# Performance work log

Measured on AMD Instinct MI355X. Metric: run time of the kernel, lower is better.

The kernel has to match this reference:

```python
import jax, jax.numpy as jnp
import numpy as np

B, L, H, NH, HD, M, NL, V, RD, NS = 4, 512, 768, 12, 64, 3072, 6, 32000, 128, 2
EPS = 1e-12
COEF = 1.0 / float(np.sqrt(HD))
NEG_INF = float('-inf')


def _ln(x, scale, bias):
    x = x - jnp.mean(x, axis=-1, keepdims=True)
    x = x * jax.lax.rsqrt(jnp.mean(jnp.square(x), axis=-1, keepdims=True) + EPS)
    return x * scale + bias


def setup_inputs() -> dict:
    key = jax.random.key(0)
    ks = jax.random.split(key, 16)
    def p(k, shape):
        return jax.random.normal(k, shape, jnp.float32) * 0.02
    return dict(
        token_ids=jax.random.randint(ks[0], (B, L), 0, V, jnp.int32),
        segment_ids=jax.random.randint(ks[1], (B, L), 0, NS, jnp.int32),
        input_mask=jnp.ones((B, L), jnp.int32),
        tok_emb=p(ks[2], (V, H)),
        seg_emb=p(ks[3], (NS, H)),
        emb_scale=jnp.ones((H,), jnp.float32),
        emb_bias=jnp.zeros((H,), jnp.float32),
        Wq=p(ks[4], (NL, H, NH, HD)), bq=jnp.zeros((NL, NH, HD), jnp.float32),
        Wk=p(ks[5], (NL, H, NH, HD)), bk=jnp.zeros((NL, NH, HD), jnp.float32),
        Wv=p(ks[6], (NL, H, NH, HD)), bv=jnp.zeros((NL, NH, HD), jnp.float32),
        relpos=p(ks[7], (NL, 2 * RD - 1, H)),
        Wo=p(ks[8], (NL, NH, HD, H)), bo=jnp.zeros((NL, H), jnp.float32),
        ln1_s=jnp.ones((NL, H), jnp.float32), ln1_b=jnp.zeros((NL, H), jnp.float32),
        W1=p(ks[9], (NL, H, M)), b1=jnp.zeros((NL, M), jnp.float32),
        W2=p(ks[10], (NL, M, H)), b2=jnp.zeros((NL, H), jnp.float32),
        ln2_s=jnp.ones((NL, H), jnp.float32), ln2_b=jnp.zeros((NL, H), jnp.float32),
    )


def _encoder(token_ids, segment_ids, input_mask,
             tok_emb, seg_emb, emb_scale, emb_bias,
             Wq, bq, Wk, bk, Wv, bv, relpos, Wo, bo,
             ln1_s, ln1_b, W1, b1, W2, b2, ln2_s, ln2_b):
    # Embedding block: token + segment embeddings, layer norm (dropout = eval/no-op)
    x = tok_emb[token_ids] + seg_emb[segment_ids]            # [B, L, H]
    x = _ln(x, emb_scale, emb_bias)
    mask = jnp.where(input_mask.astype(bool), 0.0, NEG_INF)[:, None, None, :]  # [B,1,1,L]

    for i in range(NL):
        # --- relative-position self-attention ---
        q = jnp.einsum('bqe,ehd->bqhd', x, Wq[i]) + bq[i]
        k = jnp.einsum('bke,ehd->bkhd', x, Wk[i]) + bk[i]
        v = jnp.einsum('bke,ehd->bkhd', x, Wv[i]) + bv[i]
        att = jnp.einsum('bqhd,bkhd->bhqk', q, k) + mask      # [B,NH,L,L]
        # skew trick: embed absolute [L,L] scores into relative [L, 2L-1] layout
        att = jnp.pad(att, [(0, 0), (0, 0), (0, 0), (0, L - 2)], constant_values=NEG_INF)
        att = att.reshape(att.shape[:2] + (L * (2 * L - 2),))
        att = jnp.pad(att, [(0, 0), (0, 0), (L - 1, 1)], constant_values=NEG_INF)
        att = att.reshape(att.shape[:2] + (L, 2 * L - 1))     # [B,NH,L,2L-1]
        # relative-position key/value embeddings, edge-padded to 2L-1 rows
        pad = L - RD
        rel_emb = jnp.pad(relpos[i], [(pad, pad), (0, 0)], mode='edge')  # [2L-1, H]
        k_rel = jnp.einsum('re,ehd->rhd', rel_emb, Wk[i]) + bk[i]
        att = (att + jnp.einsum('bqhd,rhd->bhqr', q, k_rel)) * COEF
        probs = jax.nn.softmax(att, axis=-1)                  # [B,NH,L,2L-1]
        v_rel = jnp.einsum('re,ehd->rhd', rel_emb, Wv[i]) + bv[i]
        rel_ctx = jnp.einsum('bhqr,rhd->bqhd', probs, v_rel)
        # un-skew probs back to [B,NH,L,L] for the absolute-position context
        p = probs.reshape(probs.shape[:2] + (L * (2 * L - 1),))[:, :, L - 1:-1]
        p = p.reshape(probs.shape[:2] + (L, 2 * L - 2))[:, :, :, :L]
        ctx = jnp.einsum('bhqk,bkhd->bqhd', p, v) + rel_ctx
        y = jnp.einsum('bqhd,hde->bqe', ctx, Wo[i]) + bo[i]
        x = _ln(x + y, ln1_s[i], ln1_b[i])
        # --- MLP block ---
        y = jax.nn.gelu(jnp.einsum('bqe,em->bqm', x, W1[i]) + b1[i])
        y = jnp.einsum('bqm,me->bqe', y, W2[i]) + b2[i]
        x = _ln(x + y, ln2_s[i], ln2_b[i])
    return x


def reference(token_ids, segment_ids, input_mask,
              tok_emb, seg_emb, emb_scale, emb_bias,
              Wq, bq, Wk, bk, Wv, bv, relpos, Wo, bo,
              ln1_s, ln1_b, W1, b1, W2, b2, ln2_s, ln2_b):
    return _encoder(token_ids, segment_ids, input_mask,
                    tok_emb, seg_emb, emb_scale, emb_bias,
                    Wq, bq, Wk, bk, Wv, bv, relpos, Wo, bo,
                    ln1_s, ln1_b, W1, b1, W2, b2, ln2_s, ln2_b)
```

## Files before the change

### kernel.cpp

```cpp
#include <hip/hip_runtime.h>
#include <hip/hip_bf16.h>
#include <math.h>

#define B_   4
#define L_   512
#define H_   768
#define NH_  12
#define HD_  64
#define M_   3072
#define NL_  6
#define RD_  128
#define NR_  255
#define ROWS (B_*L_)
#define MEXT 2304
#define COEF_ 0.125f

typedef __attribute__((ext_vector_type(8))) short bf16x8;
typedef __attribute__((ext_vector_type(4))) float f32x4;


static __device__ __forceinline__ float wave_reduce_sum(float v) {
#pragma unroll
    for (int off = 32; off > 0; off >>= 1) v += __shfl_xor(v, off, 64);
    return v;
}

static __device__ __forceinline__ float gelu_f(float x) {
    float x3 = x * x * x;
    return 0.5f * x * (1.f + tanhf(0.7978845608028654f * (x + 0.044715f * x3)));
}

static __device__ __forceinline__ unsigned short f2bfu(float v) {
    __hip_bfloat16 h = __float2bfloat16(v);
    return *(unsigned short*)&h;
}

static __device__ __forceinline__ float bfu2f(unsigned short u) {
    union { float f; unsigned int i; } x;
    x.i = ((unsigned int)u) << 16;
    return x.f;
}

static __device__ __forceinline__ void gload16(const void* g, void* l) {
    __builtin_amdgcn_global_load_lds(
        (const __attribute__((address_space(1))) void*)g,
        (__attribute__((address_space(3))) void*)l,
        16, 0, 0);
}


__global__ __launch_bounds__(256) void embed_ln_kernel(
    const int* __restrict__ tok, const int* __restrict__ seg,
    const float* __restrict__ temb, const float* __restrict__ semb,
    const float* __restrict__ sc, const float* __restrict__ bi,
    float* __restrict__ out, __hip_bfloat16* __restrict__ outb)
{
    int row = blockIdx.x;
    int t = threadIdx.x;
    int tid = tok[row], sid = seg[row];
    const float* tp = temb + (size_t)tid * H_;
    const float* sp = semb + (size_t)sid * H_;
    float v[3];
#pragma unroll
    for (int j = 0; j < 3; j++) { int idx = t + j * 256; v[j] = tp[idx] + sp[idx]; }

    __shared__ float red[4];
    __shared__ float bc;
    int lane = t & 63, wid = t >> 6;

    float s = v[0] + v[1] + v[2];
    s = wave_reduce_sum(s);
    if (lane == 0) red[wid] = s;
    __syncthreads();
    if (t == 0) bc = (red[0] + red[1] + red[2] + red[3]) * (1.f / H_);
    __syncthreads();
    float mean = bc;

    float c[3]; float ss = 0.f;
#pragma unroll
    for (int j = 0; j < 3; j++) { c[j] = v[j] - mean; ss += c[j] * c[j]; }
    ss = wave_reduce_sum(ss);
    __syncthreads();
    if (lane == 0) red[wid] = ss;
    __syncthreads();
    if (t == 0) bc = rsqrtf((red[0] + red[1] + red[2] + red[3]) * (1.f / H_) + 1e-12f);
    __syncthreads();
    float r = bc;
#pragma unroll
    for (int j = 0; j < 3; j++) {
        int idx = t + j * 256;
        float o = c[j] * r * sc[idx] + bi[idx];
        out[(size_t)row * H_ + idx] = o;
        outb[(size_t)row * H_ + idx] = __float2bfloat16(o);
    }
}


__global__ __launch_bounds__(256) void add_ln_kernel(
    const float* __restrict__ x, const float* __restrict__ p0,
    const float* __restrict__ p1, const float* __restrict__ p2,
    const float* __restrict__ bias,
    const float* __restrict__ sc, const float* __restrict__ bi,
    float* __restrict__ out, __hip_bfloat16* __restrict__ outb)
{
    int row = blockIdx.x;
    int t = threadIdx.x;
    const float* xp = x + (size_t)row * H_;
    const float* q0 = p0 + (size_t)row * H_;
    const float* q1 = p1 ? p1 + (size_t)row * H_ : nullptr;
    const float* q2 = p2 ? p2 + (size_t)row * H_ : nullptr;
    float v[3];
#pragma unroll
    for (int j = 0; j < 3; j++) {
        int idx = t + j * 256;
        float a = xp[idx] + q0[idx];
        if (q1) a += q1[idx];
        if (q2) a += q2[idx];
        if (bias) a += bias[idx];
        v[j] = a;
    }

    __shared__ float red[4];
    __shared__ float bc;
    int lane = t & 63, wid = t >> 6;

    float s = v[0] + v[1] + v[2];
    s = wave_reduce_sum(s);
    if (lane == 0) red[wid] = s;
    __syncthreads();
    if (t == 0) bc = (red[0] + red[1] + red[2] + red[3]) * (1.f / H_);
    __syncthreads();
    float mean = bc;

    float c[3]; float ss = 0.f;
#pragma unroll
    for (int j = 0; j < 3; j++) { c[j] = v[j] - mean; ss += c[j] * c[j]; }
    ss = wave_reduce_sum(ss);
    __syncthreads();
    if (lane == 0) red[wid] = ss;
    __syncthreads();
    if (t == 0) bc = rsqrtf((red[0] + red[1] + red[2] + red[3]) * (1.f / H_) + 1e-12f);
    __syncthreads();
    float r = bc;
#pragma unroll
    for (int j = 0; j < 3; j++) {
        int idx = t + j * 256;
        float o = c[j] * r * sc[idx] + bi[idx];
        out[(size_t)row * H_ + idx] = o;
        if (outb) outb[(size_t)row * H_ + idx] = __float2bfloat16(o);
    }
}


__global__ __launch_bounds__(256) void transpose_cvt_kernel(
    const float* __restrict__ in, __hip_bfloat16* __restrict__ out, int K, int N)
{
    __shared__ float tile[32][33];
    int bx = blockIdx.x * 32;
    int by = blockIdx.y * 32;
    int tx = threadIdx.x & 31, ty = threadIdx.x >> 5;
#pragma unroll
    for (int i = 0; i < 4; i++)
        tile[ty + 8 * i][tx] = in[(size_t)(by + ty + 8 * i) * N + bx + tx];
    __syncthreads();
#pragma unroll
    for (int i = 0; i < 4; i++)
        out[(size_t)(bx + ty + 8 * i) * K + by + tx] = __float2bfloat16(tile[tx][ty + 8 * i]);
}

__global__ __launch_bounds__(256) void transpose_cvt3_kernel(
    const float* __restrict__ in0, const float* __restrict__ in1, const float* __restrict__ in2,
    __hip_bfloat16* __restrict__ out)
{
    const float* in = blockIdx.z == 0 ? in0 : (blockIdx.z == 1 ? in1 : in2);
    __hip_bfloat16* o = out + (size_t)blockIdx.z * H_ * H_;
    __shared__ float tile[32][33];
    int bx = blockIdx.x * 32;
    int by = blockIdx.y * 32;
    int tx = threadIdx.x & 31, ty = threadIdx.x >> 5;
#pragma unroll
    for (int i = 0; i < 4; i++)
        tile[ty + 8 * i][tx] = in[(size_t)(by + ty + 8 * i) * H_ + bx + tx];
    __syncthreads();
#pragma unroll
    for (int i = 0; i < 4; i++)
        o[(size_t)(bx + ty + 8 * i) * H_ + by + tx] = __float2bfloat16(tile[tx][ty + 8 * i]);
}

__global__ void cvt_kernel(const float* __restrict__ in, __hip_bfloat16* __restrict__ out, int n) {
    int i = blockIdx.x * blockDim.x + threadIdx.x;
    int stride = gridDim.x * blockDim.x;
    for (; i < n; i += stride) out[i] = __float2bfloat16(in[i]);
}

__global__ void pack_qkv_bias_kernel(const float* __restrict__ bq, const float* __restrict__ bk,
                                     const float* __restrict__ bv, float* __restrict__ out) {
    int i = blockIdx.x * 256 + threadIdx.x;
    if (i >= 2304) return;
    out[i] = i < 768 ? bq[i] : (i < 1536 ? bk[i - 768] : bv[i - 1536]);
}


__global__ __launch_bounds__(256) void transpose_vvr_kernel(
    const __hip_bfloat16* __restrict__ qkvb,
    __hip_bfloat16* __restrict__ vT, __hip_bfloat16* __restrict__ vrT)
{
    __shared__ unsigned short tile[64][72];
    const int bx = blockIdx.x;
    const int h  = blockIdx.y;
    const int t = threadIdx.x;
    const int r = t >> 2, c0 = (t & 3) * 16;
    if (bx < 32) {
        const int kb = bx * 64;
        const unsigned short* src = (const unsigned short*)qkvb + (size_t)(kb + r) * 2304 + 1536 + h * 64 + c0;
        *(uint4*)&tile[r][c0]     = *(const uint4*)src;
        *(uint4*)&tile[r][c0 + 8] = *(const uint4*)(src + 8);
        __syncthreads();
        unsigned short outv[16];
#pragma unroll
        for (int i = 0; i < 16; i++) outv[i] = tile[c0 + i][r];
        unsigned short* dst = (unsigned short*)vT +
            ((size_t)((kb >> 9) * NH_ + h) * 64 + r) * 512 + (kb & 511) + c0;
        *(uint4*)dst       = *(uint4*)&outv[0];
        *(uint4*)(dst + 8) = *(uint4*)&outv[8];
    } else {
        const int jb = (bx - 32) * 64;
        const int j = jb + r;
        if (j < NR_) {
            const unsigned short* src = (const unsigned short*)qkvb + (size_t)(2048 + j) * 2304 + 1536 + h * 64 + c0;
            *(uint4*)&tile[r][c0]     = *(const uint4*)src;
            *(uint4*)&tile[r][c0 + 8] = *(const uint4*)(src + 8);
        } else {
#pragma unroll
            for (int i = 0; i < 16; i++) tile[r][c0 + i] = 0;
        }
        __syncthreads();
        unsigned short outv[16];
#pragma unroll
        for (int i = 0; i < 16; i++) outv[i] = tile[c0 + i][r];
        unsigned short* dst = (unsigned short*)vrT + ((size_t)(h * 64) + r) * 256 + jb + c0;
        *(uint4*)dst       = *(uint4*)&outv[0];
        *(uint4*)(dst + 8) = *(uint4*)&outv[8];
    }
}


#define TK 64

__global__ __launch_bounds__(512, 4) void gemm_bf16_kernel(
    const __hip_bfloat16* __restrict__ A, const __hip_bfloat16* __restrict__ Bt,
    const float* __restrict__ bias, float* __restrict__ Cf, __hip_bfloat16* __restrict__ Cb,
    float* __restrict__ CfX, size_t xstride,
    int M, int N, int K, int act, int ksplit)
{
    __shared__ __hip_bfloat16 As[2][128 * TK];
    __shared__ __hip_bfloat16 Bs[2][128 * TK];
    const int t = threadIdx.x;
    const int lane = t & 63;
    const int wid = t >> 6;
    const int lq = lane & 15, lg = lane >> 4;
    const int wm = (wid & 3) * 32, wn = (wid >> 2) * 64;

    const int nbx = gridDim.x;
    const int nwg = nbx * gridDim.y;
    int wgid = blockIdx.y * nbx + blockIdx.x;
    if ((nwg & 7) == 0) { int qq = nwg >> 3; wgid = (wgid & 7) * qq + (wgid >> 3); }
    const int bm = (wgid / nbx) * 128, bn = (wgid % nbx) * 128;
    const int kbase = blockIdx.z * ksplit;

    f32x4 acc[2][4];
#pragma unroll
    for (int i = 0; i < 2; i++)
#pragma unroll
        for (int j = 0; j < 4; j++) acc[i][j] = (f32x4){0.f, 0.f, 0.f, 0.f};

    const int rl = t >> 3;
    const int cswz = (((t & 7) * 16) ^ ((rl & 7) << 4)) >> 1;
    const __hip_bfloat16* ga[2];
    const __hip_bfloat16* gb[2];
    int lofs[2];
#pragma unroll
    for (int c = 0; c < 2; c++) {
        int rowa = bm + c * 64 + rl; if (rowa >= M) rowa = M - 1;
        int rowb = bn + c * 64 + rl;
        ga[c] = A  + (size_t)rowa * K + kbase + cswz;
        gb[c] = Bt + (size_t)rowb * K + kbase + cswz;
        lofs[c] = (c * 64 + wid * 8) * TK;
    }

    const int nt = ksplit / TK;
#pragma unroll
    for (int c = 0; c < 2; c++) {
        gload16(ga[c], &As[0][lofs[c]]);
        gload16(gb[c], &Bs[0][lofs[c]]);
    }
    __syncthreads();

    int cur = 0;
    for (int kt = 0; kt < nt; kt++) {
        if (kt + 1 < nt) {
#pragma unroll
            for (int c = 0; c < 2; c++) {
                gload16(ga[c] + (kt + 1) * TK, &As[cur ^ 1][lofs[c]]);
                gload16(gb[c] + (kt + 1) * TK, &Bs[cur ^ 1][lofs[c]]);
            }
        }
#pragma unroll
        for (int kh = 0; kh < 2; kh++) {
            const int kb = kh * 64 + lg * 16;
            bf16x8 af[2], bfr[4];
#pragma unroll
            for (int i = 0; i < 2; i++) {
                int ra = wm + i * 16 + lq;
                af[i] = *(const bf16x8*)((const char*)&As[cur][0] + ra * 128 + (kb ^ ((ra & 7) << 4)));
            }
#pragma unroll
            for (int j = 0; j < 4; j++) {
                int rb = wn + j * 16 + lq;
                bfr[j] = *(const bf16x8*)((const char*)&Bs[cur][0] + rb * 128 + (kb ^ ((rb & 7) << 4)));
            }
#pragma unroll
            for (int i = 0; i < 2; i++)
#pragma unroll
                for (int j = 0; j < 4; j++)
                    acc[i][j] = __builtin_amdgcn_mfma_f32_16x16x32_bf16(af[i], bfr[j], acc[i][j], 0, 0, 0);
        }
        __syncthreads();
        cur ^= 1;
    }

    float* outf = (blockIdx.z == 0) ? Cf : (CfX + (size_t)(blockIdx.z - 1) * xstride);
#pragma unroll
    for (int i = 0; i < 2; i++) {
#pragma unroll
        for (int j = 0; j < 4; j++) {
            int col = bn + wn + j * 16 + lq;
            float bsv = bias ? bias[col] : 0.f;
            int row0 = bm + wm + i * 16 + lg * 4;
#pragma unroll
            for (int rr = 0; rr < 4; rr++) {
                int row = row0 + rr;
                if (row >= M) continue;
                float v = acc[i][j][rr] + bsv;
                if (act) v = gelu_f(v);
                if (Cb && blockIdx.z == 0) Cb[(size_t)row * N + col] = __float2bfloat16(v);
                else                       outf[(size_t)row * N + col] = v;
            }
        }
    }
}


#define PS_LD 520
#define PR_LD 264

__global__ __launch_bounds__(256, 3) void attn_kernel(
    const __hip_bfloat16* __restrict__ qkvb,
    const __hip_bfloat16* __restrict__ vT,
    const __hip_bfloat16* __restrict__ vrT,
    const int* __restrict__ mask,
    __hip_bfloat16* __restrict__ ctxb)
{
    __shared__ unsigned short RqPrel[32 * PR_LD];
    __shared__ unsigned short Ps[32 * PS_LD];
    __shared__ float mstat[32 * 4];
    __shared__ float sstat[32 * 4];
    __shared__ float maskb[512];

    const int i_ = blockIdx.x;
    const int c_ = i_ & 7, s_ = i_ >> 3;
    const int p_ = c_ + 8 * (s_ >> 4);
    const int qt = s_ & 15;
    const int b = p_ / 12, h = p_ % 12;

    const int t = threadIdx.x;
    const int lane = t & 63, w = t >> 6;
    const int lq = lane & 15, lg = lane >> 4;

    maskb[t]       = mask[b * L_ + t]       ? 0.f : -1e30f;
    maskb[t + 256] = mask[b * L_ + t + 256] ? 0.f : -1e30f;

    const char* Qbase  = (const char*)qkvb + ((size_t)(b * L_ + qt * 32) * 2304 + h * 64) * 2;
    const char* Kbase  = (const char*)qkvb + ((size_t)(b * L_) * 2304 + 768 + h * 64) * 2;
    const char* KRbase = (const char*)qkvb + ((size_t)2048 * 2304 + 768 + h * 64) * 2;

    bf16x8 afq[2][2];
#pragma unroll
    for (int ks = 0; ks < 2; ks++) {
        const int kofs = ks * 64 + lg * 16;
        afq[ks][0] = *(const bf16x8*)(Qbase + (size_t)lq * 4608 + kofs);
        afq[ks][1] = *(const bf16x8*)(Qbase + (size_t)(16 + lq) * 4608 + kofs);
    }

    {
        f32x4 accr[2][4];
#pragma unroll
        for (int i = 0; i < 2; i++)
#pragma unroll
            for (int j = 0; j < 4; j++) accr[i][j] = (f32x4){0.f, 0.f, 0.f, 0.f};
#pragma unroll
        for (int ks = 0; ks < 2; ks++) {
            const int kofs = ks * 64 + lg * 16;
            bf16x8 bkr_[4];
#pragma unroll
            for (int jt = 0; jt < 4; jt++) {
                int j = w * 64 + jt * 16 + lq;
                int jr = j > 254 ? 254 : j;
                bkr_[jt] = *(const bf16x8*)(KRbase + (size_t)jr * 4608 + kofs);
            }
#pragma unroll
            for (int jt = 0; jt < 4; jt++) {
                accr[0][jt] = __builtin_amdgcn_mfma_f32_16x16x32_bf16(afq[ks][0], bkr_[jt], accr[0][jt], 0, 0, 0);
                accr[1][jt] = __builtin_amdgcn_mfma_f32_16x16x32_bf16(afq[ks][1], bkr_[jt], accr[1][jt], 0, 0, 0);
            }
        }
#pragma unroll
        for (int it = 0; it < 2; it++)
#pragma unroll
            for (int jt = 0; jt < 4; jt++)
#pragma unroll
                for (int r = 0; r < 4; r++)
                    RqPrel[(it * 16 + lg * 4 + r) * PR_LD + w * 64 + jt * 16 + lq] = f2bfu(accr[it][jt][r]);
    }
    __syncthreads();

    f32x4 accs[2][8];
#pragma unroll
    for (int i = 0; i < 2; i++)
#pragma unroll
        for (int j = 0; j < 8; j++) accs[i][j] = (f32x4){0.f, 0.f, 0.f, 0.f};
#pragma unroll
    for (int ks = 0; ks < 2; ks++) {
        const int kofs = ks * 64 + lg * 16;
        bf16x8 bk_[8];
#pragma unroll
        for (int jt = 0; jt < 8; jt++) {
            int key = w * 128 + jt * 16 + lq;
            bk_[jt] = *(const bf16x8*)(Kbase + (size_t)key * 4608 + kofs);
        }
#pragma unroll
        for (int jt = 0; jt < 8; jt++) {
            accs[0][jt] = __builtin_amdgcn_mfma_f32_16x16x32_bf16(afq[ks][0], bk_[jt], accs[0][jt], 0, 0, 0);
            accs[1][jt] = __builtin_amdgcn_mfma_f32_16x16x32_bf16(afq[ks][1], bk_[jt], accs[1][jt], 0, 0, 0);
        }
    }

#pragma unroll
    for (int it = 0; it < 2; it++) {
#pragma unroll
        for (int r = 0; r < 4; r++) {
            int q = it * 16 + lg * 4 + r;
            int qg = qt * 32 + q;
            float mx = -INFINITY;
#pragma unroll
            for (int jt = 0; jt < 8; jt++) {
                int k = w * 128 + jt * 16 + lq;
                int jc = k - qg + 127;
                jc = jc < 0 ? 0 : (jc > 254 ? 254 : jc);
                float s = (accs[it][jt][r] + bfu2f(RqPrel[q * PR_LD + jc])) * COEF_ + maskb[k];
                accs[it][jt][r] = s;
                mx = fmaxf(mx, s);
            }
#pragma unroll
            for (int off = 1; off < 16; off <<= 1) mx = fmaxf(mx, __shfl_xor(mx, off, 64));
            if (lq == 0) mstat[q * 4 + w] = mx;
        }
    }
    __syncthreads();

#pragma unroll
    for (int it = 0; it < 2; it++) {
#pragma unroll
        for (int r = 0; r < 4; r++) {
            int q = it * 16 + lg * 4 + r;
            float4 mv = *(const float4*)&mstat[q * 4];
            float gm = fmaxf(fmaxf(mv.x, mv.y), fmaxf(mv.z, mv.w));
            float ssum = 0.f;
#pragma unroll
            for (int jt = 0; jt < 8; jt++) {
                int k = w * 128 + jt * 16 + lq;
                float p = __expf(accs[it][jt][r] - gm);
                ssum += p;
                Ps[q * PS_LD + k] = f2bfu(p);
            }
#pragma unroll
            for (int off = 1; off < 16; off <<= 1) ssum += __shfl_xor(ssum, off, 64);
            if (lq == 0) sstat[q * 4 + w] = ssum;
        }
    }
    __syncthreads();

    const __hip_bfloat16* vTb  = vT  + (((size_t)(b * NH_ + h) * 64) + w * 16 + lq) * 512 + lg * 8;
    const __hip_bfloat16* vrTb = vrT + ((size_t)(h * 64) + w * 16 + lq) * 256 + lg * 8;
    bf16x8 bvpre[8], vrpre[8];
#pragma unroll
    for (int ks = 0; ks < 8; ks++) {
        bvpre[ks] = *(const bf16x8*)(vTb + ks * 32);
        vrpre[ks] = *(const bf16x8*)(vrTb + ks * 32);
    }
    {
        int q = t >> 3, sub = t & 7;
        int qg = qt * 32 + q;
#pragma unroll
        for (int jj = 0; jj < 32; jj++) {
            int j = sub + 8 * jj;
            if (j == 0 || j == 254) continue;
            if (j == 255) { RqPrel[q * PR_LD + 255] = 0; continue; }
            int k = qg + j - 127;
            unsigned short val = ((unsigned)k < 512u) ? Ps[q * PS_LD + k] : (unsigned short)0;
            RqPrel[q * PR_LD + j] = val;
        }
    }
    {
        int task = t >> 2, ts = t & 3;
        int q = task >> 1, side = task & 1;
        int qg = qt * 32 + q;
        float sum = 0.f;
        if (side == 0) {
            int hi = qg - 127;
            for (int k = ts; k <= hi; k += 4) sum += bfu2f(Ps[q * PS_LD + k]);
        } else {
            for (int k = qg + 127 + ts; k < 512; k += 4) sum += bfu2f(Ps[q * PS_LD + k]);
        }
        sum += __shfl_xor(sum, 1, 64);
        sum += __shfl_xor(sum, 2, 64);
        if (ts == 0) RqPrel[q * PR_LD + (side == 0 ? 0 : 254)] = f2bfu(sum);
    }
    __syncthreads();

    f32x4 accv[2];
    accv[0] = (f32x4){0.f, 0.f, 0.f, 0.f};
    accv[1] = (f32x4){0.f, 0.f, 0.f, 0.f};

#pragma unroll
    for (int ks = 0; ks < 8; ks++) {
        bf16x8 pa0 = *(const bf16x8*)((const char*)Ps + (size_t)lq * (PS_LD * 2) + ks * 64 + lg * 16);
        bf16x8 pa1 = *(const bf16x8*)((const char*)Ps + (size_t)(16 + lq) * (PS_LD * 2) + ks * 64 + lg * 16);
        accv[0] = __builtin_amdgcn_mfma_f32_16x16x32_bf16(pa0, bvpre[ks], accv[0], 0, 0, 0);
        accv[1] = __builtin_amdgcn_mfma_f32_16x16x32_bf16(pa1, bvpre[ks], accv[1], 0, 0, 0);
    }
#pragma unroll
    for (int ks = 8; ks < 16; ks++) {
        bf16x8 bv = *(const bf16x8*)(vTb + ks * 32);
        bf16x8 pa0 = *(const bf16x8*)((const char*)Ps + (size_t)lq * (PS_LD * 2) + ks * 64 + lg * 16);
        bf16x8 pa1 = *(const bf16x8*)((const char*)Ps + (size_t)(16 + lq) * (PS_LD * 2) + ks * 64 + lg * 16);
        accv[0] = __builtin_amdgcn_mfma_f32_16x16x32_bf16(pa0, bv, accv[0], 0, 0, 0);
        accv[1] = __builtin_amdgcn_mfma_f32_16x16x32_bf16(pa1, bv, accv[1], 0, 0, 0);
    }
#pragma unroll
    for (int ks = 0; ks < 8; ks++) {
        bf16x8 pa0 = *(const bf16x8*)((const char*)RqPrel + (size_t)lq * (PR_LD * 2) + ks * 64 + lg * 16);
        bf16x8 pa1 = *(const bf16x8*)((const char*)RqPrel + (size_t)(16 + lq) * (PR_LD * 2) + ks * 64 + lg * 16);
        accv[0] = __builtin_amdgcn_mfma_f32_16x16x32_bf16(pa0, vrpre[ks], accv[0], 0, 0, 0);
        accv[1] = __builtin_amdgcn_mfma_f32_16x16x32_bf16(pa1, vrpre[ks], accv[1], 0, 0, 0);
    }

#pragma unroll
    for (int it = 0; it < 2; it++) {
#pragma unroll
        for (int r = 0; r < 4; r++) {
            int q = it * 16 + lg * 4 + r;
            float4 sv = *(const float4*)&sstat[q * 4];
            float inv = 1.f / (sv.x + sv.y + sv.z + sv.w);
            ctxb[(size_t)(b * L_ + qt * 32 + q) * 768 + h * 64 + w * 16 + lq] =
                __float2bfloat16(accv[it][r] * inv);
        }
    }
}


extern "C" void kernel_launch(void* const* d_in, const int* in_sizes, int n_in,
                              void* d_out, int out_size, void* d_ws, size_t ws_size,
                              hipStream_t stream)
{
    const int*   tok    = (const int*)d_in[0];
    const int*   seg    = (const int*)d_in[1];
    const int*   maskp  = (const int*)d_in[2];
    const float* temb   = (const float*)d_in[3];
    const float* semb   = (const float*)d_in[4];
    const float* esc    = (const float*)d_in[5];
    const float* ebi    = (const float*)d_in[6];
    const float* Wq     = (const float*)d_in[7];
    const float* bq     = (const float*)d_in[8];
    const float* Wk     = (const float*)d_in[9];
    const float* bk     = (const float*)d_in[10];
    const float* Wv     = (const float*)d_in[11];
    const float* bv     = (const float*)d_in[12];
    const float* relpos = (const float*)d_in[13];
    const float* Wo     = (const float*)d_in[14];
    const float* bo     = (const float*)d_in[15];
    const float* ln1s   = (const float*)d_in[16];
    const float* ln1b   = (const float*)d_in[17];
    const float* W1     = (const float*)d_in[18];
    const float* b1     = (const float*)d_in[19];
    const float* W2     = (const float*)d_in[20];
    const float* b2     = (const float*)d_in[21];
    const float* ln2s   = (const float*)d_in[22];
    const float* ln2b   = (const float*)d_in[23];

    const size_t NX = (size_t)ROWS * H_;
    float* x       = (float*)d_ws;
    float* x2      = x + NX;
    float* y       = x2 + NX;
    float* qkvbias = y + NX;
    __hip_bfloat16* xb    = (__hip_bfloat16*)(qkvbias + 2304);
    __hip_bfloat16* x2b   = xb    + (size_t)MEXT * H_;
    __hip_bfloat16* ctxb  = x2b   + NX;
    __hip_bfloat16* qkvb  = ctxb  + NX;
    __hip_bfloat16* vT    = qkvb  + (size_t)MEXT * 2304;
    __hip_bfloat16* vrT   = vT    + (size_t)B_ * NH_ * 64 * 512;
    __hip_bfloat16* Wt    = vrT   + (size_t)NH_ * 64 * 256;
    __hip_bfloat16* h1b   = Wt    + (size_t)M_ * H_;

    float* spill = (float*)qkvb;

    dim3 blk(256);
    dim3 blk512(512);

    embed_ln_kernel<<<ROWS, blk, 0, stream>>>(tok, seg, temb, semb, esc, ebi, x, xb);

    for (int l = 0; l < NL_; l++) {
        const float* wq = Wq + (size_t)l * H_ * H_;
        const float* wk = Wk + (size_t)l * H_ * H_;
        const float* wv = Wv + (size_t)l * H_ * H_;
        const float* wo = Wo + (size_t)l * H_ * H_;
        const float* w1 = W1 + (size_t)l * H_ * M_;
        const float* w2 = W2 + (size_t)l * M_ * H_;

        transpose_cvt3_kernel<<<dim3(24, 24, 3), blk, 0, stream>>>(wq, wk, wv, Wt);
        pack_qkv_bias_kernel<<<9, blk, 0, stream>>>(bq + (size_t)l * H_, bk + (size_t)l * H_, bv + (size_t)l * H_, qkvbias);
        cvt_kernel<<<192, blk, 0, stream>>>(relpos + (size_t)l * NR_ * H_, xb + (size_t)ROWS * H_, NR_ * H_);

        gemm_bf16_kernel<<<dim3(18, 18), blk512, 0, stream>>>(xb, Wt, qkvbias, nullptr, qkvb, nullptr, 0,
                                                              MEXT, 2304, H_, 0, H_);
        transpose_vvr_kernel<<<dim3(36, 12), blk, 0, stream>>>(qkvb, vT, vrT);

        attn_kernel<<<dim3(768), blk, 0, stream>>>(qkvb, vT, vrT, maskp, ctxb);

        transpose_cvt_kernel<<<dim3(24, 24), blk, 0, stream>>>(wo, Wt, H_, H_);
        gemm_bf16_kernel<<<dim3(6, 16, 2), blk512, 0, stream>>>(ctxb, Wt, nullptr, y, nullptr, spill, NX,
                                                                ROWS, H_, H_, 0, 384);
        add_ln_kernel<<<ROWS, blk, 0, stream>>>(x, y, spill, nullptr, bo + (size_t)l * H_,
                                                ln1s + (size_t)l * H_, ln1b + (size_t)l * H_, x2, x2b);

        transpose_cvt_kernel<<<dim3(96, 24), blk, 0, stream>>>(w1, Wt, H_, M_);
        gemm_bf16_kernel<<<dim3(24, 16), blk512, 0, stream>>>(x2b, Wt, b1 + (size_t)l * M_, nullptr, h1b, nullptr, 0,
                                                              ROWS, M_, H_, 1, H_);
        transpose_cvt_kernel<<<dim3(24, 96), blk, 0, stream>>>(w2, Wt, M_, H_);
        gemm_bf16_kernel<<<dim3(6, 16, 3), blk512, 0, stream>>>(h1b, Wt, nullptr, y, nullptr, spill, NX,
                                                                ROWS, H_, M_, 0, 1024);

        float* outp = (l == NL_ - 1) ? (float*)d_out : x;
        __hip_bfloat16* outbp = (l == NL_ - 1) ? nullptr : xb;
        add_ln_kernel<<<ROWS, blk, 0, stream>>>(x2, y, spill, spill + NX, b2 + (size_t)l * H_,
                                                ln2s + (size_t)l * H_, ln2b + (size_t)l * H_, outp, outbp);
    }
}
```

Before: 899.4 us.

## Merge per-layer weight packing into one kernel and halve GEMM N-tile

All per-layer weight transposes/conversions, bias packing and relpos conversion are merged into a single launch writing to separate weight buffers, removing several small kernel launches and the serialization between the shared Wt buffer and each GEMM. The GEMM tile shrinks from 128x128 to 128x64 with launch bounds raised to 6 waves/SIMD target, doubling grid sizes to improve CU occupancy for these small GEMMs. The smaller tile lowers data reuse per block and increases B-operand loads relative to compute, and more workspace is needed for the separate weight buffers.

Result: faster. 732.0 us, median of 2 (-18.6%).

```diff
diff --git a/kernel.cpp b/kernel.cpp
--- a/kernel.cpp
+++ b/kernel.cpp
@@ -152,52 +152,52 @@
 }
 
 
-__global__ __launch_bounds__(256) void transpose_cvt_kernel(
-    const float* __restrict__ in, __hip_bfloat16* __restrict__ out, int K, int N)
+__global__ __launch_bounds__(256) void pack_layer_kernel(
+    const float* __restrict__ wq, const float* __restrict__ wk, const float* __restrict__ wv,
+    const float* __restrict__ wo, const float* __restrict__ w1, const float* __restrict__ w2,
+    const float* __restrict__ bqL, const float* __restrict__ bkL, const float* __restrict__ bvL,
+    const float* __restrict__ relL,
+    __hip_bfloat16* __restrict__ WtQ, __hip_bfloat16* __restrict__ WtO,
+    __hip_bfloat16* __restrict__ WtW1, __hip_bfloat16* __restrict__ WtW2,
+    float* __restrict__ qkvbias, __hip_bfloat16* __restrict__ relb)
 {
+    const int z = blockIdx.z;
+    const int t = threadIdx.x;
+    if (z == 6) {
+        int id = blockIdx.y * 96 + blockIdx.x;
+        if (id < 765) {
+            int i = id * 256 + t;
+            relb[i] = __float2bfloat16(relL[i]);
+        } else if (id < 774) {
+            int i = (id - 765) * 256 + t;
+            if (i < 2304)
+                qkvbias[i] = i < 768 ? bqL[i] : (i < 1536 ? bkL[i - 768] : bvL[i - 1536]);
+        }
+        return;
+    }
+    const float* in; __hip_bfloat16* out; int K, N;
+    int bx = blockIdx.x, by = blockIdx.y;
+    if (z < 4) {
+        if (bx >= 24) return;
+        K = 768; N = 768;
+        in = (z == 0) ? wq : (z == 1) ? wk : (z == 2) ? wv : wo;
+        out = (z < 3) ? WtQ + (size_t)z * H_ * H_ : WtO;
+    } else if (z == 4) {
+        K = 768; N = 3072; in = w1; out = WtW1;
+    } else {
+        K = 3072; N = 768; in = w2; out = WtW2;
+        int tmp = bx; bx = by; by = tmp;
+    }
     __shared__ float tile[32][33];
-    int bx = blockIdx.x * 32;
-    int by = blockIdx.y * 32;
-    int tx = threadIdx.x & 31, ty = threadIdx.x >> 5;
+    int bX = bx * 32, bY = by * 32;
+    int tx = t & 31, ty = t >> 5;
 #pragma unroll
     for (int i = 0; i < 4; i++)
-        tile[ty + 8 * i][tx] = in[(size_t)(by + ty + 8 * i) * N + bx + tx];
+        tile[ty + 8 * i][tx] = in[(size_t)(bY + ty + 8 * i) * N + bX + tx];
     __syncthreads();
 #pragma unroll
     for (int i = 0; i < 4; i++)
-        out[(size_t)(bx + ty + 8 * i) * K + by + tx] = __float2bfloat16(tile[tx][ty + 8 * i]);
-}
-
-__global__ __launch_bounds__(256) void transpose_cvt3_kernel(
-    const float* __restrict__ in0, const float* __restrict__ in1, const float* __restrict__ in2,
-    __hip_bfloat16* __restrict__ out)
-{
-    const float* in = blockIdx.z == 0 ? in0 : (blockIdx.z == 1 ? in1 : in2);
-    __hip_bfloat16* o = out + (size_t)blockIdx.z * H_ * H_;
-    __shared__ float tile[32][33];
-    int bx = blockIdx.x * 32;
-    int by = blockIdx.y * 32;
-    int tx = threadIdx.x & 31, ty = threadIdx.x >> 5;
-#pragma unroll
-    for (int i = 0; i < 4; i++)
-        tile[ty + 8 * i][tx] = in[(size_t)(by + ty + 8 * i) * H_ + bx + tx];
-    __syncthreads();
-#pragma unroll
-    for (int i = 0; i < 4; i++)
-        o[(size_t)(bx + ty + 8 * i) * H_ + by + tx] = __float2bfloat16(tile[tx][ty + 8 * i]);
-}
-
-__global__ void cvt_kernel(const float* __restrict__ in, __hip_bfloat16* __restrict__ out, int n) {
-    int i = blockIdx.x * blockDim.x + threadIdx.x;
-    int stride = gridDim.x * blockDim.x;
-    for (; i < n; i += stride) out[i] = __float2bfloat16(in[i]);
-}
-
-__global__ void pack_qkv_bias_kernel(const float* __restrict__ bq, const float* __restrict__ bk,
-                                     const float* __restrict__ bv, float* __restrict__ out) {
-    int i = blockIdx.x * 256 + threadIdx.x;
-    if (i >= 2304) return;
-    out[i] = i < 768 ? bq[i] : (i < 1536 ? bk[i - 768] : bv[i - 1536]);
+        out[(size_t)(bX + ty + 8 * i) * K + bY + tx] = __float2bfloat16(tile[tx][ty + 8 * i]);
 }
 
 
@@ -247,82 +247,79 @@
 
 #define TK 64
 
-__global__ __launch_bounds__(512, 4) void gemm_bf16_kernel(
+__global__ __launch_bounds__(512, 6) void gemm_bf16_kernel(
     const __hip_bfloat16* __restrict__ A, const __hip_bfloat16* __restrict__ Bt,
     const float* __restrict__ bias, float* __restrict__ Cf, __hip_bfloat16* __restrict__ Cb,
     float* __restrict__ CfX, size_t xstride,
     int M, int N, int K, int act, int ksplit)
 {
     __shared__ __hip_bfloat16 As[2][128 * TK];
-    __shared__ __hip_bfloat16 Bs[2][128 * TK];
+    __shared__ __hip_bfloat16 Bs[2][64 * TK];
     const int t = threadIdx.x;
     const int lane = t & 63;
     const int wid = t >> 6;
     const int lq = lane & 15, lg = lane >> 4;
-    const int wm = (wid & 3) * 32, wn = (wid >> 2) * 64;
+    const int wm = (wid & 3) * 32, wn = (wid >> 2) * 32;
 
     const int nbx = gridDim.x;
     const int nwg = nbx * gridDim.y;
     int wgid = blockIdx.y * nbx + blockIdx.x;
     if ((nwg & 7) == 0) { int qq = nwg >> 3; wgid = (wgid & 7) * qq + (wgid >> 3); }
-    const int bm = (wgid / nbx) * 128, bn = (wgid % nbx) * 128;
+    const int bm = (wgid / nbx) * 128, bn = (wgid % nbx) * 64;
     const int kbase = blockIdx.z * ksplit;
 
-    f32x4 acc[2][4];
+    f32x4 acc[2][2];
 #pragma unroll
     for (int i = 0; i < 2; i++)
 #pragma unroll
-        for (int j = 0; j < 4; j++) acc[i][j] = (f32x4){0.f, 0.f, 0.f, 0.f};
+        for (int j = 0; j < 2; j++) acc[i][j] = (f32x4){0.f, 0.f, 0.f, 0.f};
 
     const int rl = t >> 3;
     const int cswz = (((t & 7) * 16) ^ ((rl & 7) << 4)) >> 1;
     const __hip_bfloat16* ga[2];
-    const __hip_bfloat16* gb[2];
-    int lofs[2];
+    const __hip_bfloat16* gb;
+    int lofsA[2], lofsB;
 #pragma unroll
     for (int c = 0; c < 2; c++) {
         int rowa = bm + c * 64 + rl; if (rowa >= M) rowa = M - 1;
-        int rowb = bn + c * 64 + rl;
-        ga[c] = A  + (size_t)rowa * K + kbase + cswz;
-        gb[c] = Bt + (size_t)rowb * K + kbase + cswz;
-        lofs[c] = (c * 64 + wid * 8) * TK;
-    }
+        ga[c] = A + (size_t)rowa * K + kbase + cswz;
+        lofsA[c] = (c * 64 + wid * 8) * TK;
+    }
+    gb = Bt + (size_t)(bn + rl) * K + kbase + cswz;
+    lofsB = (wid * 8) * TK;
 
     const int nt = ksplit / TK;
-#pragma unroll
-    for (int c = 0; c < 2; c++) {
-        gload16(ga[c], &As[0][lofs[c]]);
-        gload16(gb[c], &Bs[0][lofs[c]]);
-    }
+    gload16(ga[0], &As[0][lofsA[0]]);
+    gload16(ga[1], &As[0][lofsA[1]]);
+    gload16(gb,    &Bs[0][lofsB]);
     __syncthreads();
 
     int cur = 0;
     for (int kt = 0; kt < nt; kt++) {
         if (kt + 1 < nt) {
-#pragma unroll
-            for (int c = 0; c < 2; c++) {
-                gload16(ga[c] + (kt + 1) * TK, &As[cur ^ 1][lofs[c]]);
-                gload16(gb[c] + (kt + 1) * TK, &Bs[cur ^ 1][lofs[c]]);
-            }
+            const int koff = (kt + 1) * TK;
+            gload16(ga[0] + koff, &As[cur ^ 1][lofsA[0]]);
+            gload16(ga[1] + koff, &As[cur ^ 1][lofsA[1]]);
+            gload16(gb + koff,    &Bs[cur ^ 1][lofsB]);
         }
 #pragma unroll
         for (int kh = 0; kh < 2; kh++) {
             const int kb = kh * 64 + lg * 16;
-            bf16x8 af[2], bfr[4];
+            bf16x8 af[2], bfr[2];
 #pragma unroll
             for (int i = 0; i < 2; i++) {
                 int ra = wm + i * 16 + lq;
                 af[i] = *(const bf16x8*)((const char*)&As[cur][0] + ra * 128 + (kb ^ ((ra & 7) << 4)));
             }
 #pragma unroll
-            for (int j = 0; j < 4; j++) {
+            for (int j = 0; j < 2; j++) {
                 int rb = wn + j * 16 + lq;
                 bfr[j] = *(const bf16x8*)((const char*)&Bs[cur][0] + rb * 128 + (kb ^ ((rb & 7) << 4)));
             }
 #pragma unroll
             for (int i = 0; i < 2; i++)
 #pragma unroll
-                for (int j = 0; j < 4; j++)
+                for (int j = 0; j < 2; j++)
                     acc[i][j] = __builtin_amdgcn_mfma_f32_16x16x32_bf16(af[i], bfr[j], acc[i][j], 0, 0, 0);
         }
         __syncthreads();
@@ -333,7 +330,7 @@
 #pragma unroll
     for (int i = 0; i < 2; i++) {
 #pragma unroll
-        for (int j = 0; j < 4; j++) {
+        for (int j = 0; j < 2; j++) {
             int col = bn + wn + j * 16 + lq;
             float bsv = bias ? bias[col] : 0.f;
             int row0 = bm + wm + i * 16 + lg * 4;
@@ -609,8 +606,11 @@
     __hip_bfloat16* qkvb  = ctxb  + NX;
     __hip_bfloat16* vT    = qkvb  + (size_t)MEXT * 2304;
     __hip_bfloat16* vrT   = vT    + (size_t)B_ * NH_ * 64 * 512;
-    __hip_bfloat16* Wt    = vrT   + (size_t)NH_ * 64 * 256;
-    __hip_bfloat16* h1b   = Wt    + (size_t)M_ * H_;
+    __hip_bfloat16* WtQ   = vrT   + (size_t)NH_ * 64 * 256;
+    __hip_bfloat16* WtO   = WtQ   + (size_t)2304 * H_;
+    __hip_bfloat16* WtW1  = WtO   + (size_t)H_ * H_;
+    __hip_bfloat16* WtW2  = WtW1  + (size_t)M_ * H_;
+    __hip_bfloat16* h1b   = WtW2  + (size_t)H_ * M_;
 
     float* spill = (float*)qkvb;
 
@@ -627,28 +627,27 @@
         const float* w1 = W1 + (size_t)l * H_ * M_;
         const float* w2 = W2 + (size_t)l * M_ * H_;
 
-        transpose_cvt3_kernel<<<dim3(24, 24, 3), blk, 0, stream>>>(wq, wk, wv, Wt);
-        pack_qkv_bias_kernel<<<9, blk, 0, stream>>>(bq + (size_t)l * H_, bk + (size_t)l * H_, bv + (size_t)l * H_, qkvbias);
-        cvt_kernel<<<192, blk, 0, stream>>>(relpos + (size_t)l * NR_ * H_, xb + (size_t)ROWS * H_, NR_ * H_);
-
-        gemm_bf16_kernel<<<dim3(18, 18), blk512, 0, stream>>>(xb, Wt, qkvbias, nullptr, qkvb, nullptr, 0,
+        pack_layer_kernel<<<dim3(96, 24, 7), blk, 0, stream>>>(
+            wq, wk, wv, wo, w1, w2,
+            bq + (size_t)l * H_, bk + (size_t)l * H_, bv + (size_t)l * H_,
+            relpos + (size_t)l * NR_ * H_,
+            WtQ, WtO, WtW1, WtW2, qkvbias, xb + (size_t)ROWS * H_);
+
+        gemm_bf16_kernel<<<dim3(36, 18), blk512, 0, stream>>>(xb, WtQ, qkvbias, nullptr, qkvb, nullptr, 0,
                                                               MEXT, 2304, H_, 0, H_);
         transpose_vvr_kernel<<<dim3(36, 12), blk, 0, stream>>>(qkvb, vT, vrT);
 
         attn_kernel<<<dim3(768), blk, 0, stream>>>(qkvb, vT, vrT, maskp, ctxb);
 
-        transpose_cvt_kernel<<<dim3(24, 24), blk, 0, stream>>>(wo, Wt, H_, H_);
-        gemm_bf16_kernel<<<dim3(6, 16, 2), blk512, 0, stream>>>(ctxb, Wt, nullptr, y, nullptr, spill, NX,
-                                                                ROWS, H_, H_, 0, 384);
+        gemm_bf16_kernel<<<dim3(12, 16, 2), blk512, 0, stream>>>(ctxb, WtO, nullptr, y, nullptr, spill, NX,
+                                                                 ROWS, H_, H_, 0, 384);
         add_ln_kernel<<<ROWS, blk, 0, stream>>>(x, y, spill, nullptr, bo + (size_t)l * H_,
                                                 ln1s + (size_t)l * H_, ln1b + (size_t)l * H_, x2, x2b);
 
-        transpose_cvt_kernel<<<dim3(96, 24), blk, 0, stream>>>(w1, Wt, H_, M_);
-        gemm_bf16_kernel<<<dim3(24, 16), blk512, 0, stream>>>(x2b, Wt, b1 + (size_t)l * M_, nullptr, h1b, nullptr, 0,
+        gemm_bf16_kernel<<<dim3(48, 16), blk512, 0, stream>>>(x2b, WtW1, b1 + (size_t)l * M_, nullptr, h1b, nullptr, 0,
                                                               ROWS, M_, H_, 1, H_);
-        transpose_cvt_kernel<<<dim3(24, 96), blk, 0, stream>>>(w2, Wt, M_, H_);
-        gemm_bf16_kernel<<<dim3(6, 16, 3), blk512, 0, stream>>>(h1b, Wt, nullptr, y, nullptr, spill, NX,
-                                                                ROWS, H_, M_, 0, 1024);
+        gemm_bf16_kernel<<<dim3(12, 16, 3), blk512, 0, stream>>>(h1b, WtW2, nullptr, y, nullptr, spill, NX,
+                                                                 ROWS, H_, M_, 0, 1024);
 
         float* outp = (l == NL_ - 1) ? (float*)d_out : x;
         __hip_bfloat16* outbp = (l == NL_ - 1) ? nullptr : xb;
```
